# Kernel optimization log

Hardware: AMD Instinct MI355X
Metric: run time of the kernel (lower is better)

The kernel has to match this reference:

```python
import jax, jax.numpy as jnp
import numpy as np

N_QUBITS = 20
BATCH = 16


def setup_inputs() -> dict:
    key = jax.random.key(0)
    k1, k2 = jax.random.split(key)
    phi = jax.random.normal(k1, (BATCH, 2 ** N_QUBITS), dtype=jnp.float32)
    thetas = jax.random.normal(k2, (BATCH, N_QUBITS), dtype=jnp.float32)
    return {"phi": phi, "thetas": thetas}


def reference(phi, thetas):
    """Apply per-qubit RX(theta) rotations to the state vector.

    phi: [B, 2**n] real float32 initial amplitudes (cast to complex64).
    thetas: [B, n] rotation angles, qubit 0 = most-significant bit
    (matches torch view([B] + [2]*n) axis ordering, applied sequentially).
    Returns real/imag stacked: [B, 2**n, 2] float32.
    """
    B, S = phi.shape
    n = N_QUBITS
    c = jnp.cos(thetas / 2).astype(jnp.complex64)          # [B, n]
    s = (-1j * jnp.sin(thetas / 2)).astype(jnp.complex64)  # [B, n]
    state = phi.astype(jnp.complex64)                      # [B, S]
    for i in range(n):  # fixed small loop over qubits (butterfly stages)
        left = 2 ** i
        right = S // (2 * left)
        st = state.reshape(B, left, 2, right)
        a = st[:, :, 0, :]
        b = st[:, :, 1, :]
        ci = c[:, i, None, None]
        si = s[:, i, None, None]
        na = ci * a + si * b
        nb = si * a + ci * b
        state = jnp.stack([na, nb], axis=2).reshape(B, S)
    return jnp.stack([state.real, state.imag], axis=-1)
```

## Files before the change

### kernel.cpp

```cpp
#include <hip/hip_runtime.h>
#include <hip/hip_fp16.h>

#define NQ 20

__device__ __forceinline__ float bcast_first(float x) {
    return __int_as_float(__builtin_amdgcn_readfirstlane(__float_as_int(x)));
}

__device__ __forceinline__ void bfly(float C, float SV, float2& a, float2& b) {
    float2 na = make_float2(C * a.x + SV * b.y, C * a.y - SV * b.x);
    float2 nb = make_float2(C * b.x + SV * a.y, C * b.y - SV * a.x);
    a = na; b = nb;
}

__device__ __forceinline__ void bfly4(float C, float SV, float4& a, float4& b) {
    float4 na = make_float4(C*a.x + SV*b.y, C*a.y - SV*b.x, C*a.z + SV*b.w, C*a.w - SV*b.z);
    float4 nb = make_float4(C*b.x + SV*a.y, C*b.y - SV*a.x, C*b.z + SV*a.w, C*b.w - SV*a.z);
    a = na; b = nb;
}

__device__ __forceinline__ unsigned int pack_h2(float re, float im) {
    __half2 h = __floats2half2_rn(re, im);
    return *(unsigned int*)&h;
}
__device__ __forceinline__ float2 unpack_h2(unsigned int u) {
    return __half22float2(*(__half2*)&u);
}

__device__ __forceinline__ int swz1(int l) { return l ^ (((l >> 7) & 7) << 2); }

__global__ void rx_trig(const float* __restrict__ thetas, float2* __restrict__ tab) {
    int i = threadIdx.x;
    if (i < 16 * NQ) {
        float th = 0.5f * thetas[i];
        tab[i] = make_float2(cosf(th), sinf(th));
    }
}

__global__ __launch_bounds__(64) void rx_pass1_h(
        const float* __restrict__ phi, const float2* __restrict__ tab,
        unsigned int* __restrict__ ws) {
    __shared__ unsigned int lds[2048];
    const int lane = threadIdx.x;
    const int W = blockIdx.x;
    const int b = W >> 9;
    const int base = (W & 511) << 11;
    const float* ph = phi + ((size_t)b << NQ) + base;
    unsigned int* wp = ws + ((size_t)b << NQ) + base;

    float c[11], sv[11];
#pragma unroll
    for (int beta = 0; beta < 11; ++beta) {
        float2 t = tab[b * NQ + (NQ - 1 - beta)];
        c[beta]  = bcast_first(t.x);
        sv[beta] = bcast_first(t.y);
    }

    float2 v[32];
#pragma unroll
    for (int k4 = 0; k4 < 8; ++k4) {
        float4 t = *(const float4*)(ph + (k4 << 8) + (lane << 2));
        v[k4 * 4 + 0] = make_float2(t.x, 0.f);
        v[k4 * 4 + 1] = make_float2(t.y, 0.f);
        v[k4 * 4 + 2] = make_float2(t.z, 0.f);
        v[k4 * 4 + 3] = make_float2(t.w, 0.f);
    }

    const int regbit1[5]  = {0, 1, 8, 9, 10};
    const int regmask1[5] = {1, 2, 4, 8, 16};
#pragma unroll
    for (int t = 0; t < 5; ++t) {
        const float C = c[regbit1[t]], SV = sv[regbit1[t]];
        const int m = regmask1[t];
#pragma unroll
        for (int r = 0; r < 32; ++r)
            if (!(r & m)) bfly(C, SV, v[r], v[r | m]);
    }

#pragma unroll
    for (int k4 = 0; k4 < 8; ++k4) {
        int low0 = (k4 << 8) + (lane << 2);
        int s0 = swz1(low0);
        uint4 pk;
        pk.x = pack_h2(v[k4*4+0].x, v[k4*4+0].y);
        pk.y = pack_h2(v[k4*4+1].x, v[k4*4+1].y);
        pk.z = pack_h2(v[k4*4+2].x, v[k4*4+2].y);
        pk.w = pack_h2(v[k4*4+3].x, v[k4*4+3].y);
        *(uint4*)&lds[s0] = pk;
    }
    __syncthreads();

    {
        const int g = lane >> 2, lam = lane & 3;
        float2 w2[32];
#pragma unroll
        for (int r = 0; r < 32; ++r) {
            int l = (g << 7) | (r << 2) | lam;
            w2[r] = unpack_h2(lds[swz1(l)]);
        }
#pragma unroll
        for (int t = 0; t < 5; ++t) {
            const float C = c[2 + t], SV = sv[2 + t];
            const int m = 1 << t;
#pragma unroll
            for (int r = 0; r < 32; ++r)
                if (!(r & m)) bfly(C, SV, w2[r], w2[r | m]);
        }
#pragma unroll
        for (int r = 0; r < 32; ++r) {
            int l = (g << 7) | (r << 2) | lam;
            lds[swz1(l)] = pack_h2(w2[r].x, w2[r].y);
        }
    }
    __syncthreads();

    float2 u2[32];
#pragma unroll
    for (int m = 0; m < 16; ++m) {
        int l0 = ((m & 1) << 1) | ((lane & 31) << 2) | (((m >> 1) & 1) << 7)
               | (((lane >> 5) & 1) << 8) | (((m >> 2) & 3) << 9);
        uint2 t = *(uint2*)&lds[swz1(l0)];
        u2[2*m]     = unpack_h2(t.x);
        u2[2*m + 1] = unpack_h2(t.y);
    }
    {
        const float C = c[7], SV = sv[7];
#pragma unroll
        for (int m = 0; m < 16; ++m)
            if (!(m & 2)) {
                bfly(C, SV, u2[2*m],     u2[2*(m|2)]);
                bfly(C, SV, u2[2*m + 1], u2[2*(m|2) + 1]);
            }
    }
#pragma unroll
    for (int k = 0; k < 8; ++k) {
        int X = ((lane & 31) << 2) | ((k & 1) << 7)
              | (((lane >> 5) & 1) << 8) | ((k >> 1) << 9);
        uint4 pk;
        pk.x = pack_h2(u2[4*k + 0].x, u2[4*k + 0].y);
        pk.y = pack_h2(u2[4*k + 1].x, u2[4*k + 1].y);
        pk.z = pack_h2(u2[4*k + 2].x, u2[4*k + 2].y);
        pk.w = pack_h2(u2[4*k + 3].x, u2[4*k + 3].y);
        *(uint4*)(wp + X) = pk;
    }
}

__device__ __forceinline__ int p2idx(int h, int g) {
    return (h << 5) + (((g ^ (h & 7)) & 7) << 2);
}

__global__ __launch_bounds__(512, 4) void rx_pass2_h(
        const float2* __restrict__ tab, const unsigned int* __restrict__ ws,
        float2* __restrict__ out) {
    __shared__ unsigned int buf[16384];
    const int tid = threadIdx.x;
    const int b = blockIdx.x >> 6;
    const int lb = blockIdx.x & 63;
    const unsigned int* pin = ws + ((size_t)b << NQ) + (lb << 5);
    float2* pout = out + ((size_t)b << NQ) + (lb << 5);

    float c[9], sv[9];
#pragma unroll
    for (int i = 0; i < 9; ++i) {
        float2 t = tab[b * NQ + (8 - i)];
        c[i]  = bcast_first(t.x);
        sv[i] = bcast_first(t.y);
    }

#pragma unroll
    for (int i = 0; i < 8; ++i) {
        int f = (i << 9) | tid;
        int h = f >> 3, q = f & 7;
        uint4 t = *(const uint4*)(pin + h * 2048 + (q << 2));
        *(uint4*)&buf[p2idx(h, q)] = t;
    }
    __syncthreads();

    {
        const int hl = tid & 31;
        const int j  = tid >> 5;
        const int g = j >> 1, off = (j & 1) << 1;
        float4 w[16];
#pragma unroll
        for (int m = 0; m < 16; ++m) {
            int h = (m << 5) | hl;
            uint2 t = *(const uint2*)&buf[p2idx(h, g) + off];
            float2 a = unpack_h2(t.x), bb = unpack_h2(t.y);
            w[m] = make_float4(a.x, a.y, bb.x, bb.y);
        }
#pragma unroll
        for (int t = 0; t < 4; ++t) {
            const float C = c[5 + t], SV = sv[5 + t];
            const int msk = 1 << t;
#pragma unroll
            for (int m = 0; m < 16; ++m)
                if (!(m & msk)) bfly4(C, SV, w[m], w[m | msk]);
        }
#pragma unroll
        for (int m = 0; m < 16; ++m) {
            int h = (m << 5) | hl;
            uint2 t;
            t.x = pack_h2(w[m].x, w[m].y);
            t.y = pack_h2(w[m].z, w[m].w);
            *(uint2*)&buf[p2idx(h, g) + off] = t;
        }
    }
    __syncthreads();

    {
        const int hh = tid >> 5;
        const int ll = tid & 31;
        const int g = ll >> 2, off = ll & 3;
        float2 v[32];
#pragma unroll
        for (int r = 0; r < 32; ++r) {
            int h = (hh << 5) | r;
            v[r] = unpack_h2(buf[p2idx(h, g) + off]);
        }
#pragma unroll
        for (int t = 0; t < 5; ++t) {
            const float C = c[t], SV = sv[t];
            const int msk = 1 << t;
#pragma unroll
            for (int r = 0; r < 32; ++r)
                if (!(r & msk)) bfly(C, SV, v[r], v[r | msk]);
        }
#pragma unroll
        for (int r = 0; r < 32; ++r) {
            int h = (hh << 5) | r;
            pout[h * 2048 + ll] = v[r];
        }
    }
}

__global__ __launch_bounds__(64) void rx_pass1(
        const float* __restrict__ phi, const float* __restrict__ thetas,
        float2* __restrict__ out) {
    __shared__ float2 lds[2048];
    const int lane = threadIdx.x;
    const int W = blockIdx.x;
    const int b = W >> 9;
    const int base = (W & 511) << 11;
    const float* ph = phi + ((size_t)b << NQ) + base;
    float2* op = out + ((size_t)b << NQ) + base;

    float c[11], sv[11];
#pragma unroll
    for (int beta = 0; beta < 11; ++beta) {
        float th = 0.5f * thetas[b * NQ + (NQ - 1 - beta)];
        c[beta]  = bcast_first(cosf(th));
        sv[beta] = bcast_first(sinf(th));
    }

    float2 v[32];
#pragma unroll
    for (int k4 = 0; k4 < 8; ++k4) {
        float4 t = *(const float4*)(ph + (k4 << 8) + (lane << 2));
        v[k4 * 4 + 0] = make_float2(t.x, 0.f);
        v[k4 * 4 + 1] = make_float2(t.y, 0.f);
        v[k4 * 4 + 2] = make_float2(t.z, 0.f);
        v[k4 * 4 + 3] = make_float2(t.w, 0.f);
    }

    const int regbit1[5]  = {0, 1, 8, 9, 10};
    const int regmask1[5] = {1, 2, 4, 8, 16};
#pragma unroll
    for (int t = 0; t < 5; ++t) {
        const float C = c[regbit1[t]], SV = sv[regbit1[t]];
        const int m = regmask1[t];
#pragma unroll
        for (int r = 0; r < 32; ++r)
            if (!(r & m)) bfly(C, SV, v[r], v[r | m]);
    }

#pragma unroll
    for (int k4 = 0; k4 < 8; ++k4) {
        int low0 = (k4 << 8) + (lane << 2);
        int s0 = swz1(low0);
        *(float4*)&lds[s0]     = make_float4(v[k4*4+0].x, v[k4*4+0].y, v[k4*4+1].x, v[k4*4+1].y);
        *(float4*)&lds[s0 + 2] = make_float4(v[k4*4+2].x, v[k4*4+2].y, v[k4*4+3].x, v[k4*4+3].y);
    }
    __syncthreads();

    {
        const int g = lane >> 2, lam = lane & 3;
        float2 w2[32];
#pragma unroll
        for (int r = 0; r < 32; ++r) {
            int l = (g << 7) | (r << 2) | lam;
            w2[r] = lds[swz1(l)];
        }
#pragma unroll
        for (int t = 0; t < 5; ++t) {
            const float C = c[2 + t], SV = sv[2 + t];
            const int m = 1 << t;
#pragma unroll
            for (int r = 0; r < 32; ++r)
                if (!(r & m)) bfly(C, SV, w2[r], w2[r | m]);
        }
#pragma unroll
        for (int r = 0; r < 32; ++r) {
            int l = (g << 7) | (r << 2) | lam;
            lds[swz1(l)] = w2[r];
        }
    }
    __syncthreads();

    float4 u[16];
#pragma unroll
    for (int m = 0; m < 16; ++m) {
        int l0 = (lane << 1) | ((m & 1) << 7) | (((m >> 1) & 1) << 8)
               | (((m >> 2) & 1) << 9) | (((m >> 3) & 1) << 10);
        u[m] = *(float4*)&lds[swz1(l0)];
    }
    {
        const float C = c[7], SV = sv[7];
#pragma unroll
        for (int m = 0; m < 16; m += 2) {
            float4 A = u[m], B = u[m + 1];
            u[m]     = make_float4(C*A.x + SV*B.y, C*A.y - SV*B.x, C*A.z + SV*B.w, C*A.w - SV*B.z);
            u[m + 1] = make_float4(C*B.x + SV*A.y, C*B.y - SV*A.x, C*B.z + SV*A.w, C*B.w - SV*A.z);
        }
    }
#pragma unroll
    for (int m = 0; m < 16; ++m) {
        int l0 = (lane << 1) | ((m & 1) << 7) | (((m >> 1) & 1) << 8)
               | (((m >> 2) & 1) << 9) | (((m >> 3) & 1) << 10);
        *(float4*)(op + l0) = u[m];
    }
}

__device__ __forceinline__ int ppos(int h, int q) {
    return (h << 4) + (((q ^ (h & 7) ^ ((h >> 5) & 7)) & 7) << 1);
}

__global__ __launch_bounds__(256) void rx_pass2(
        const float* __restrict__ thetas, float2* __restrict__ out) {
    __shared__ float2 buf[8192];
    const int tid = threadIdx.x;
    const int b = blockIdx.x >> 7;
    const int lb = blockIdx.x & 127;
    float2* p = out + ((size_t)b << NQ) + (lb << 4);

    float c[9], sv[9];
#pragma unroll
    for (int i = 0; i < 9; ++i) {
        float th = 0.5f * thetas[b * NQ + (8 - i)];
        c[i]  = bcast_first(cosf(th));
        sv[i] = bcast_first(sinf(th));
    }

#pragma unroll
    for (int i = 0; i < 16; ++i) {
        int f = (i << 8) | tid;
        int h = f >> 3, j = f & 7;
        float4 t = *(const float4*)(p + h * 2048 + (j << 1));
        *(float4*)&buf[ppos(h, j)] = t;
    }
    __syncthreads();

    {
        const int hl = tid & 31;
        const int j  = tid >> 5;
        float4 w[16];
#pragma unroll
        for (int m = 0; m < 16; ++m)
            w[m] = *(float4*)&buf[ppos((m << 5) | hl, j)];
#pragma unroll
        for (int t = 0; t < 4; ++t) {
            const float C = c[5 + t], SV = sv[5 + t];
            const int msk = 1 << t;
#pragma unroll
            for (int m = 0; m < 16; ++m)
                if (!(m & msk)) bfly4(C, SV, w[m], w[m | msk]);
        }
#pragma unroll
        for (int m = 0; m < 16; ++m)
            *(float4*)&buf[ppos((m << 5) | hl, j)] = w[m];
    }
    __syncthreads();

    {
        const int hh = tid >> 4;
        const int ll = tid & 15;
        float2 v[32];
#pragma unroll
        for (int r = 0; r < 32; ++r) {
            int h = (hh << 5) | r;
            v[r] = buf[ppos(h, ll >> 1) + (ll & 1)];
        }
#pragma unroll
        for (int t = 0; t < 5; ++t) {
            const float C = c[t], SV = sv[t];
            const int msk = 1 << t;
#pragma unroll
            for (int r = 0; r < 32; ++r)
                if (!(r & msk)) bfly(C, SV, v[r], v[r | msk]);
        }
#pragma unroll
        for (int r = 0; r < 32; ++r) {
            int h = (hh << 5) | r;
            p[h * 2048 + ll] = v[r];
        }
    }
}

extern "C" void kernel_launch(void* const* d_in, const int* in_sizes, int n_in,
                              void* d_out, int out_size, void* d_ws, size_t ws_size,
                              hipStream_t stream) {
    const float* phi    = (const float*)d_in[0];
    const float* thetas = (const float*)d_in[1];
    float2* out = (float2*)d_out;
    const size_t half_bytes = ((size_t)16 << NQ) * 4;
    const size_t need = half_bytes + 4096;
    if (d_ws != nullptr && ws_size >= need) {
        unsigned int* ws = (unsigned int*)d_ws;
        float2* tab = (float2*)((char*)d_ws + half_bytes);
        rx_trig<<<1, 320, 0, stream>>>(thetas, tab);
        rx_pass1_h<<<8192, 64, 0, stream>>>(phi, tab, ws);
        rx_pass2_h<<<1024, 512, 0, stream>>>(tab, ws, out);
    } else {
        rx_pass1<<<8192, 64, 0, stream>>>(phi, thetas, out);
        rx_pass2<<<2048, 256, 0, stream>>>(thetas, out);
    }
}
```

Before: 266.2 us.

## Merge pass1 LDS stages with shuffle butterfly and widen pass2 tiles

In pass1, the second LDS round-trip and its barrier are removed. The stage-7 butterfly now runs through cross-lane shuffles in registers, and the final store copies straight from LDS to global memory. Pass2 doubles its tile to 64 columns with 1024-thread blocks and a 128 KB shared buffer, using a wider swizzle, to get longer contiguous global accesses. The larger blocks may lower occupancy because the launch bounds ask for 4 blocks of 1024 threads that LDS likely cannot hold.

```diff
diff --git a/kernel.cpp b/kernel.cpp
--- a/kernel.cpp
+++ b/kernel.cpp
@@ -79,8 +79,7 @@
 
 #pragma unroll
     for (int k4 = 0; k4 < 8; ++k4) {
-        int low0 = (k4 << 8) + (lane << 2);
-        int s0 = swz1(low0);
+        int s0 = swz1((k4 << 8) + (lane << 2));
         uint4 pk;
         pk.x = pack_h2(v[k4*4+0].x, v[k4*4+0].y);
         pk.y = pack_h2(v[k4*4+1].x, v[k4*4+1].y);
@@ -90,74 +89,57 @@
     }
     __syncthreads();
 
-    {
-        const int g = lane >> 2, lam = lane & 3;
-        float2 w2[32];
-#pragma unroll
-        for (int r = 0; r < 32; ++r) {
-            int l = (g << 7) | (r << 2) | lam;
-            w2[r] = unpack_h2(lds[swz1(l)]);
-        }
-#pragma unroll
-        for (int t = 0; t < 5; ++t) {
-            const float C = c[2 + t], SV = sv[2 + t];
-            const int m = 1 << t;
-#pragma unroll
-            for (int r = 0; r < 32; ++r)
-                if (!(r & m)) bfly(C, SV, w2[r], w2[r | m]);
-        }
-#pragma unroll
-        for (int r = 0; r < 32; ++r) {
-            int l = (g << 7) | (r << 2) | lam;
-            lds[swz1(l)] = pack_h2(w2[r].x, w2[r].y);
-        }
-    }
-    __syncthreads();
-
-    float2 u2[32];
-#pragma unroll
-    for (int m = 0; m < 16; ++m) {
-        int l0 = ((m & 1) << 1) | ((lane & 31) << 2) | (((m >> 1) & 1) << 7)
-               | (((lane >> 5) & 1) << 8) | (((m >> 2) & 3) << 9);
-        uint2 t = *(uint2*)&lds[swz1(l0)];
-        u2[2*m]     = unpack_h2(t.x);
-        u2[2*m + 1] = unpack_h2(t.y);
-    }
+    const int g = lane >> 2, lam = lane & 3;
+#pragma unroll
+    for (int r = 0; r < 32; ++r)
+        v[r] = unpack_h2(lds[swz1((g << 7) | (r << 2) | lam)]);
+
+#pragma unroll
+    for (int t = 0; t < 5; ++t) {
+        const float C = c[2 + t], SV = sv[2 + t];
+        const int m = 1 << t;
+#pragma unroll
+        for (int r = 0; r < 32; ++r)
+            if (!(r & m)) bfly(C, SV, v[r], v[r | m]);
+    }
+
     {
         const float C = c[7], SV = sv[7];
 #pragma unroll
-        for (int m = 0; m < 16; ++m)
-            if (!(m & 2)) {
-                bfly(C, SV, u2[2*m],     u2[2*(m|2)]);
-                bfly(C, SV, u2[2*m + 1], u2[2*(m|2) + 1]);
-            }
-    }
+        for (int r = 0; r < 32; ++r) {
+            float px = __shfl_xor(v[r].x, 4, 64);
+            float py = __shfl_xor(v[r].y, 4, 64);
+            v[r] = make_float2(C * v[r].x + SV * py, C * v[r].y - SV * px);
+        }
+    }
+
+#pragma unroll
+    for (int r = 0; r < 32; ++r)
+        lds[swz1((g << 7) | (r << 2) | lam)] = pack_h2(v[r].x, v[r].y);
+    __syncthreads();
+
 #pragma unroll
     for (int k = 0; k < 8; ++k) {
-        int X = ((lane & 31) << 2) | ((k & 1) << 7)
-              | (((lane >> 5) & 1) << 8) | ((k >> 1) << 9);
-        uint4 pk;
-        pk.x = pack_h2(u2[4*k + 0].x, u2[4*k + 0].y);
-        pk.y = pack_h2(u2[4*k + 1].x, u2[4*k + 1].y);
-        pk.z = pack_h2(u2[4*k + 2].x, u2[4*k + 2].y);
-        pk.w = pack_h2(u2[4*k + 3].x, u2[4*k + 3].y);
-        *(uint4*)(wp + X) = pk;
+        int l0 = ((lane & 31) << 2) | ((k & 1) << 7)
+               | ((lane >> 5) << 8) | ((k >> 1) << 9);
+        uint4 pk = *(uint4*)&lds[swz1(l0)];
+        *(uint4*)(wp + l0) = pk;
     }
 }
 
 __device__ __forceinline__ int p2idx(int h, int g) {
-    return (h << 5) + (((g ^ (h & 7)) & 7) << 2);
-}
-
-__global__ __launch_bounds__(512, 4) void rx_pass2_h(
+    return (h << 6) + (((g ^ (h & 15)) & 15) << 2);
+}
+
+__global__ __launch_bounds__(1024, 4) void rx_pass2_h(
         const float2* __restrict__ tab, const unsigned int* __restrict__ ws,
         float2* __restrict__ out) {
-    __shared__ unsigned int buf[16384];
+    __shared__ unsigned int buf[32768];
     const int tid = threadIdx.x;
-    const int b = blockIdx.x >> 6;
-    const int lb = blockIdx.x & 63;
-    const unsigned int* pin = ws + ((size_t)b << NQ) + (lb << 5);
-    float2* pout = out + ((size_t)b << NQ) + (lb << 5);
+    const int b = blockIdx.x >> 5;
+    const int lb = blockIdx.x & 31;
+    const unsigned int* pin = ws + ((size_t)b << NQ) + (lb << 6);
+    float2* pout = out + ((size_t)b << NQ) + (lb << 6);
 
     float c[9], sv[9];
 #pragma unroll
@@ -169,8 +151,8 @@
 
 #pragma unroll
     for (int i = 0; i < 8; ++i) {
-        int f = (i << 9) | tid;
-        int h = f >> 3, q = f & 7;
+        int f = (i << 10) | tid;
+        int h = f >> 4, q = f & 15;
         uint4 t = *(const uint4*)(pin + h * 2048 + (q << 2));
         *(uint4*)&buf[p2idx(h, q)] = t;
     }
@@ -179,12 +161,12 @@
     {
         const int hl = tid & 31;
         const int j  = tid >> 5;
-        const int g = j >> 1, off = (j & 1) << 1;
+        const int gg = j >> 1, off = (j & 1) << 1;
         float4 w[16];
 #pragma unroll
         for (int m = 0; m < 16; ++m) {
             int h = (m << 5) | hl;
-            uint2 t = *(const uint2*)&buf[p2idx(h, g) + off];
+            uint2 t = *(const uint2*)&buf[p2idx(h, gg) + off];
             float2 a = unpack_h2(t.x), bb = unpack_h2(t.y);
             w[m] = make_float4(a.x, a.y, bb.x, bb.y);
         }
@@ -202,20 +184,20 @@
             uint2 t;
             t.x = pack_h2(w[m].x, w[m].y);
             t.y = pack_h2(w[m].z, w[m].w);
-            *(uint2*)&buf[p2idx(h, g) + off] = t;
-        }
-    }
-    __syncthreads();
-
-    {
-        const int hh = tid >> 5;
-        const int ll = tid & 31;
-        const int g = ll >> 2, off = ll & 3;
+            *(uint2*)&buf[p2idx(h, gg) + off] = t;
+        }
+    }
+    __syncthreads();
+
+    {
+        const int hh = tid >> 6;
+        const int ll = tid & 63;
+        const int gg = ll >> 2, off = ll & 3;
         float2 v[32];
 #pragma unroll
         for (int r = 0; r < 32; ++r) {
             int h = (hh << 5) | r;
-            v[r] = unpack_h2(buf[p2idx(h, g) + off]);
+            v[r] = unpack_h2(buf[p2idx(h, gg) + off]);
         }
 #pragma unroll
         for (int t = 0; t < 5; ++t) {
@@ -418,7 +400,7 @@
         float2* tab = (float2*)((char*)d_ws + half_bytes);
         rx_trig<<<1, 320, 0, stream>>>(thetas, tab);
         rx_pass1_h<<<8192, 64, 0, stream>>>(phi, tab, ws);
-        rx_pass2_h<<<1024, 512, 0, stream>>>(tab, ws, out);
+        rx_pass2_h<<<512, 1024, 0, stream>>>(tab, ws, out);
     } else {
         rx_pass1<<<8192, 64, 0, stream>>>(phi, thetas, out);
         rx_pass2<<<2048, 256, 0, stream>>>(thetas, out);
```

New measurement: 278.6 us. 4.6% more time.
